# Performance work log

Hardware: AMD Instinct MI355X
Metric: run time of the kernel (lower is better)

## Reference

```python
import jax, jax.numpy as jnp
import numpy as np


def _layer_norm(x, g, b, eps=1e-5):
    mu = jnp.mean(x, axis=-1, keepdims=True)
    var = jnp.mean((x - mu) ** 2, axis=-1, keepdims=True)
    return (x - mu) * jax.lax.rsqrt(var + eps) * g + b


def setup_inputs() -> dict:
    key = jax.random.key(0)
    ks = jax.random.split(key, 12)
    L, D, HD, F, V, MAXLEN, B, S = 4, 1024, 64, 4096, 32000, 2048, 2, 1024
    s = 0.02
    return {
        "x": jax.random.randint(ks[0], (B, S), 0, V, dtype=jnp.int32),
        "tok_emb": jax.random.normal(ks[1], (V, D), jnp.float32) * s,
        "pos_emb": jax.random.normal(ks[2], (MAXLEN, D), jnp.float32) * s,
        "wq": jax.random.normal(ks[3], (L, HD, HD), jnp.float32) * s,
        "wk": jax.random.normal(ks[4], (L, HD, HD), jnp.float32) * s,
        "wv": jax.random.normal(ks[5], (L, HD, HD), jnp.float32) * s,
        "wo": jax.random.normal(ks[6], (L, D, D), jnp.float32) * s,
        "bo": jnp.zeros((L, D), jnp.float32),
        "ln1_g": jnp.ones((L, D), jnp.float32),
        "ln1_b": jnp.zeros((L, D), jnp.float32),
        "ln2_g": jnp.ones((L, D), jnp.float32),
        "ln2_b": jnp.zeros((L, D), jnp.float32),
        "w1": jax.random.normal(ks[7], (L, F, D), jnp.float32) * s,
        "b1": jnp.zeros((L, F), jnp.float32),
        "w2": jax.random.normal(ks[8], (L, D, F), jnp.float32) * s,
        "b2": jnp.zeros((L, D), jnp.float32),
        "out_w": jax.random.normal(ks[9], (V, D), jnp.float32) * s,
        "out_b": jnp.zeros((V,), jnp.float32),
    }


def reference(x, tok_emb, pos_emb, wq, wk, wv, wo, bo, ln1_g, ln1_b, ln2_g, ln2_b, w1, b1, w2, b2, out_w, out_b):
    B, S = x.shape
    D = tok_emb.shape[1]
    HD = wq.shape[-1]
    H = D // HD
    inv_scale = 1.0 / jnp.sqrt(jnp.asarray(D, jnp.float32))  # note: embed_size, not head_dim

    h = tok_emb[x] + pos_emb[:S][None]  # [B,S,D]; dropout is identity in eval

    def block(h, p):
        pwq, pwk, pwv, pwo, pbo, g1, be1, g2, be2, pw1, pb1, pw2, pb2 = p
        xh = h.reshape(B, S, H, HD)
        # per-head Linear with shared [HD,HD] weight: y = x @ W.T
        q = jnp.einsum('bshd,ed->bshe', xh, pwq)
        k = jnp.einsum('bshd,ed->bshe', xh, pwk)
        v = jnp.einsum('bshd,ed->bshe', xh, pwv)
        energy = jnp.einsum('bqhd,bkhd->bhqk', q, k)  # full [B,H,S,S] scores
        attn = jax.nn.softmax(energy * inv_scale, axis=-1)
        o = jnp.einsum('bhqk,bkhd->bqhd', attn, v).reshape(B, S, D)
        o = o @ pwo.T + pbo
        x1 = _layer_norm(o + h, g1, be1)
        ff = jax.nn.gelu(x1 @ pw1.T + pb1, approximate=False) @ pw2.T + pb2
        return _layer_norm(ff + x1, g2, be2), None

    h, _ = jax.lax.scan(block, h, (wq, wk, wv, wo, bo, ln1_g, ln1_b, ln2_g, ln2_b, w1, b1, w2, b2))
    return h @ out_w.T + out_b  # [B,S,V] logits
```

## Files before the change

kernel.cpp:

```cpp
#include <hip/hip_runtime.h>
#include <math.h>

typedef float f32x4 __attribute__((ext_vector_type(4)));
typedef unsigned short u16x8 __attribute__((ext_vector_type(8)));
typedef unsigned short u16x4 __attribute__((ext_vector_type(4)));
typedef __bf16 bf16x8 __attribute__((ext_vector_type(8)));
typedef unsigned int u32;

#define DEV static __device__ __forceinline__

DEV unsigned short f2bf(float f) {
  __bf16 h = (__bf16)f;
  return __builtin_bit_cast(unsigned short, h);
}
DEV float bf2f(unsigned short s) { return __uint_as_float(((unsigned)s) << 16); }
DEV bf16x8 asbf(u16x8 v) { return __builtin_bit_cast(bf16x8, v); }

DEV void gload16(const void* g, void* l) {
  __builtin_amdgcn_global_load_lds((const __attribute__((address_space(1))) u32*)g,
                                   (__attribute__((address_space(3))) u32*)l, 16, 0, 0);
}

__global__ void cvt_kernel(const float* __restrict__ in, unsigned short* __restrict__ out, int n8) {
  for (int i = blockIdx.x * 256 + threadIdx.x; i < n8; i += gridDim.x * 256) {
    const float* s = in + (size_t)i * 8;
    f32x4 a = *(const f32x4*)s, b = *(const f32x4*)(s + 4);
    u16x8 o;
    for (int j = 0; j < 4; ++j) { o[j] = f2bf(a[j]); o[j + 4] = f2bf(b[j]); }
    *(u16x8*)(out + (size_t)i * 8) = o;
  }
}

__global__ void cvt2_kernel(const float* __restrict__ s0, unsigned short* __restrict__ d0, int na,
                            const float* __restrict__ s1, unsigned short* __restrict__ d1, int nb) {
  int total = na + nb;
  for (int i = blockIdx.x * 256 + threadIdx.x; i < total; i += gridDim.x * 256) {
    const float* s; unsigned short* d; int k;
    if (i < na) { s = s0; d = d0; k = i; } else { s = s1; d = d1; k = i - na; }
    f32x4 a = *(const f32x4*)(s + (size_t)k * 8), b = *(const f32x4*)(s + (size_t)k * 8 + 4);
    u16x8 o;
    for (int j = 0; j < 4; ++j) { o[j] = f2bf(a[j]); o[j + 4] = f2bf(b[j]); }
    *(u16x8*)(d + (size_t)k * 8) = o;
  }
}

__global__ void cvt3q_kernel(const float* __restrict__ s0, unsigned short* __restrict__ d0,
                             const float* __restrict__ s1, unsigned short* __restrict__ d1,
                             const float* __restrict__ s2, unsigned short* __restrict__ d2) {
  int i = blockIdx.x * 256 + threadIdx.x;
  if (i >= 6144) return;
  const float* s; unsigned short* d; int k = i & 2047;
  int seg = i >> 11;
  s = (seg == 0) ? s0 : (seg == 1) ? s1 : s2;
  d = (seg == 0) ? d0 : (seg == 1) ? d1 : d2;
  f32x4 a = *(const f32x4*)(s + (size_t)k * 8), b = *(const f32x4*)(s + (size_t)k * 8 + 4);
  u16x8 o;
  for (int j = 0; j < 4; ++j) { o[j] = f2bf(a[j]); o[j + 4] = f2bf(b[j]); }
  *(u16x8*)(d + (size_t)k * 8) = o;
}

__global__ void embed_kernel(const int* __restrict__ x, const float* __restrict__ tok,
                             const float* __restrict__ pos, float* __restrict__ h,
                             unsigned short* __restrict__ hbf) {
  int t = blockIdx.x, tid = threadIdx.x;
  int v = x[t], s = t & 1023;
  f32x4 a = *(const f32x4*)(tok + (size_t)v * 1024 + tid * 4);
  f32x4 b = *(const f32x4*)(pos + (size_t)s * 1024 + tid * 4);
  f32x4 r = a + b;
  *(f32x4*)(h + (size_t)t * 1024 + tid * 4) = r;
  u16x4 rb;
  for (int i = 0; i < 4; ++i) rb[i] = f2bf(r[i]);
  *(u16x4*)(hbf + (size_t)t * 1024 + tid * 4) = rb;
}

__global__ __launch_bounds__(256) void ln_kernel(const float* __restrict__ preA,
    const float* __restrict__ preB, const float* __restrict__ res,
    const float* __restrict__ g, const float* __restrict__ bta,
    float* __restrict__ outf, unsigned short* __restrict__ outbf) {
  int row = blockIdx.x, tid = threadIdx.x;
  size_t base = (size_t)row * 1024 + tid * 4;
  f32x4 xv = *(const f32x4*)(preA + base);
  xv += *(const f32x4*)(preB + base);
  xv += *(const f32x4*)(res + base);
  float s = xv[0] + xv[1] + xv[2] + xv[3];
  float s2 = xv[0]*xv[0] + xv[1]*xv[1] + xv[2]*xv[2] + xv[3]*xv[3];
  for (int m = 1; m < 64; m <<= 1) { s += __shfl_xor(s, m); s2 += __shfl_xor(s2, m); }
  __shared__ float red[8];
  int w = tid >> 6;
  if ((tid & 63) == 0) { red[w * 2] = s; red[w * 2 + 1] = s2; }
  __syncthreads();
  s = red[0] + red[2] + red[4] + red[6];
  s2 = red[1] + red[3] + red[5] + red[7];
  float mu = s * (1.f / 1024.f);
  float var = s2 * (1.f / 1024.f) - mu * mu;
  float rs = rsqrtf(var + 1e-5f);
  f32x4 gv = *(const f32x4*)(g + tid * 4);
  f32x4 bv = *(const f32x4*)(bta + tid * 4);
  f32x4 o; u16x4 ob;
  for (int i = 0; i < 4; ++i) { o[i] = (xv[i] - mu) * rs * gv[i] + bv[i]; ob[i] = f2bf(o[i]); }
  *(f32x4*)(outf + base) = o;
  *(u16x4*)(outbf + base) = ob;
}

__global__ __launch_bounds__(256) void qkvt_kernel(const unsigned short* __restrict__ hbf,
    const unsigned short* __restrict__ wqb, const unsigned short* __restrict__ wkb,
    const unsigned short* __restrict__ wvb,
    unsigned short* __restrict__ q, unsigned short* __restrict__ k,
    unsigned short* __restrict__ vt) {
  __shared__ unsigned short T[64 * 72];
  int tid = threadIdx.x, ln = tid & 63, w = tid >> 6;
  int l15 = ln & 15, lg = ln >> 4;
  int st = blockIdx.x, hh = blockIdx.y;
  int t0 = st * 64 + w * 16;
  const unsigned short* xp = hbf + (size_t)(t0 + l15) * 1024 + hh * 64 + lg * 8;
  bf16x8 xa0 = asbf(*(const u16x8*)xp);
  bf16x8 xa1 = asbf(*(const u16x8*)(xp + 32));
  const unsigned short* wp[3] = {wqb, wkb, wvb};
  f32x4 acc[3][4] = {};
#pragma unroll
  for (int m = 0; m < 3; ++m) {
    __builtin_amdgcn_s_setprio(1);
#pragma unroll
    for (int ni = 0; ni < 4; ++ni) {
      const unsigned short* wb = wp[m] + (size_t)(ni * 16 + l15) * 64 + lg * 8;
      bf16x8 w0 = asbf(*(const u16x8*)wb);
      bf16x8 w1 = asbf(*(const u16x8*)(wb + 32));
      acc[m][ni] = __builtin_amdgcn_mfma_f32_16x16x32_bf16(xa0, w0, acc[m][ni], 0, 0, 0);
      acc[m][ni] = __builtin_amdgcn_mfma_f32_16x16x32_bf16(xa1, w1, acc[m][ni], 0, 0, 0);
    }
    __builtin_amdgcn_s_setprio(0);
  }
  unsigned short* outp[2] = {q, k};
#pragma unroll
  for (int m = 0; m < 2; ++m)
#pragma unroll
    for (int ni = 0; ni < 4; ++ni)
#pragma unroll
      for (int r = 0; r < 4; ++r)
        outp[m][(size_t)(t0 + 4 * lg + r) * 1024 + hh * 64 + ni * 16 + l15] = f2bf(acc[m][ni][r]);
#pragma unroll
  for (int ni = 0; ni < 4; ++ni)
#pragma unroll
    for (int r = 0; r < 4; ++r)
      T[(ni * 16 + l15) * 72 + (w * 16 + 4 * lg + r)] = f2bf(acc[2][ni][r]);
  __syncthreads();
  int b = st >> 4, sb = (st & 15) * 64;
#pragma unroll
  for (int j = 0; j < 2; ++j) {
    int idx = tid + 256 * j; int e = idx >> 3, s8 = (idx & 7) * 8;
    *(u16x8*)(vt + ((size_t)((b * 16 + hh) * 64 + e)) * 1024 + sb + s8) =
        *(const u16x8*)&T[e * 72 + s8];
  }
}

__global__ __launch_bounds__(256, 2) void attn_kernel(const unsigned short* __restrict__ qb,
    const unsigned short* __restrict__ kb, const unsigned short* __restrict__ vtb,
    unsigned short* __restrict__ ob) {
  constexpr int PK = 72, PV = 136, PP = 136;
  __shared__ unsigned short Ks[128 * PK], Vs[64 * PV], Ps[4][16 * PP];
  int tid = threadIdx.x, lane = tid & 63, w = tid >> 6;
  int l15 = lane & 15, lg = lane >> 4;
  int qt = blockIdx.x, bh = blockIdx.y, b = bh >> 4, hh = bh & 15;
  int q0 = qt * 64 + w * 16;
  const unsigned short* qrow = qb + ((size_t)(b * 1024 + q0 + l15) * 16 + hh) * 64 + lg * 8;
  bf16x8 qa0 = asbf(*(const u16x8*)qrow);
  bf16x8 qa1 = asbf(*(const u16x8*)(qrow + 32));
  {
    const __bf16 s = (__bf16)0.03125f;
#pragma unroll
    for (int i = 0; i < 8; ++i) { qa0[i] = qa0[i] * s; qa1[i] = qa1[i] * s; }
  }
  float m_[4] = {-1e30f, -1e30f, -1e30f, -1e30f};
  float ls[4] = {0.f, 0.f, 0.f, 0.f};
  f32x4 oacc[4] = {};

  u16x8 KR[4], VR[4];
  auto loadT = [&](int kt) {
#pragma unroll
    for (int j = 0; j < 4; ++j) {
      int idx = tid + 256 * j;
      int r = idx >> 3, c0 = (idx & 7) * 8;
      KR[j] = *(const u16x8*)(kb + ((size_t)(b * 1024 + kt * 128 + r) * 16 + hh) * 64 + c0);
      int rv = idx >> 4, cv = (idx & 15) * 8;
      VR[j] = *(const u16x8*)(vtb + ((size_t)((b * 16 + hh) * 64) + rv) * 1024 + kt * 128 + cv);
    }
  };
  auto writeT = [&]() {
#pragma unroll
    for (int j = 0; j < 4; ++j) {
      int idx = tid + 256 * j;
      int r = idx >> 3, c0 = (idx & 7) * 8;
      *(u16x8*)(&Ks[r * PK + c0]) = KR[j];
      int rv = idx >> 4, cv = (idx & 15) * 8;
      *(u16x8*)(&Vs[rv * PV + cv]) = VR[j];
    }
  };
  loadT(0); writeT();
  __syncthreads();

  for (int kt = 0; kt < 8; ++kt) {
    f32x4 sf[8] = {};
    __builtin_amdgcn_s_setprio(1);
#pragma unroll
    for (int n = 0; n < 8; ++n) {
      bf16x8 k0 = asbf(*(const u16x8*)(&Ks[(n * 16 + l15) * PK + lg * 8]));
      bf16x8 k1 = asbf(*(const u16x8*)(&Ks[(n * 16 + l15) * PK + 32 + lg * 8]));
      sf[n] = __builtin_amdgcn_mfma_f32_16x16x32_bf16(qa0, k0, sf[n], 0, 0, 0);
      sf[n] = __builtin_amdgcn_mfma_f32_16x16x32_bf16(qa1, k1, sf[n], 0, 0, 0);
    }
    __builtin_amdgcn_s_setprio(0);
    if (kt < 7) loadT(kt + 1);
    float tm[4];
#pragma unroll
    for (int r = 0; r < 4; ++r) {
      float t0 = fmaxf(fmaxf(fmaxf(sf[0][r], sf[1][r]), fmaxf(sf[2][r], sf[3][r])),
                       fmaxf(fmaxf(sf[4][r], sf[5][r]), fmaxf(sf[6][r], sf[7][r])));
      for (int msk = 1; msk < 16; msk <<= 1) t0 = fmaxf(t0, __shfl_xor(t0, msk));
      tm[r] = t0;
    }
    bool need = false;
#pragma unroll
    for (int r = 0; r < 4; ++r) need |= (tm[r] > m_[r] + 8.f);
    if (__any(need)) {
#pragma unroll
      for (int r = 0; r < 4; ++r) {
        float nm = fmaxf(m_[r], tm[r]);
        float sc = __expf(m_[r] - nm);
        ls[r] *= sc;
#pragma unroll
        for (int n = 0; n < 4; ++n) oacc[n][r] *= sc;
        m_[r] = nm;
      }
    }
    float rsum[4] = {0.f, 0.f, 0.f, 0.f};
    unsigned short pb[8][4];
#pragma unroll
    for (int n = 0; n < 8; ++n)
#pragma unroll
      for (int r = 0; r < 4; ++r) {
        float pv = __expf(sf[n][r] - m_[r]);
        rsum[r] += pv;
        pb[n][r] = f2bf(pv);
      }
#pragma unroll
    for (int r = 0; r < 4; ++r) {
      float t0 = rsum[r];
      for (int msk = 1; msk < 16; msk <<= 1) t0 += __shfl_xor(t0, msk);
      ls[r] += t0;
    }
    unsigned short* pw = Ps[w];
#pragma unroll
    for (int n = 0; n < 8; ++n)
#pragma unroll
      for (int r = 0; r < 4; ++r)
        pw[(4 * lg + r) * PP + n * 16 + l15] = pb[n][r];
    asm volatile("s_waitcnt lgkmcnt(0)" ::: "memory");
    __builtin_amdgcn_sched_barrier(0);
    bf16x8 pa[4];
#pragma unroll
    for (int ks = 0; ks < 4; ++ks)
      pa[ks] = asbf(*(const u16x8*)(&pw[l15 * PP + ks * 32 + lg * 8]));
    __builtin_amdgcn_s_setprio(1);
#pragma unroll
    for (int n = 0; n < 4; ++n) {
#pragma unroll
      for (int ks = 0; ks < 4; ++ks) {
        bf16x8 v0 = asbf(*(const u16x8*)(&Vs[(n * 16 + l15) * PV + ks * 32 + lg * 8]));
        oacc[n] = __builtin_amdgcn_mfma_f32_16x16x32_bf16(pa[ks], v0, oacc[n], 0, 0, 0);
      }
    }
    __builtin_amdgcn_s_setprio(0);
    __syncthreads();
    if (kt < 7) { writeT(); __syncthreads(); }
  }
#pragma unroll
  for (int n = 0; n < 4; ++n)
#pragma unroll
    for (int r = 0; r < 4; ++r) {
      float o = oacc[n][r] / ls[r];
      ob[((size_t)(b * 1024 + q0 + 4 * lg + r) * 16 + hh) * 64 + n * 16 + l15] = f2bf(o);
    }
}

template <int BM, int KSPLIT, int EPI>
__global__ __launch_bounds__(256) void gemm_kernel(
    const unsigned short* __restrict__ A, int lda,
    const unsigned short* __restrict__ B, int ldb,
    const float* __restrict__ bias,
    float* __restrict__ CfA, float* __restrict__ CfB, unsigned short* __restrict__ Cb,
    int ldc, int Ksub) {
  constexpr int LOGMT = (BM == 128) ? 4 : 5;
  constexpr int MT = 2048 / BM;
  constexpr int MI = BM / 32;
  __shared__ alignas(16) char smem[33280];
  unsigned short* As = (unsigned short*)smem;
  unsigned short* Bs = As + 2 * BM * 32;
  float* Cs = (float*)smem;

  int wg = blockIdx.x;
  int mt = wg & (MT - 1);
  int rest = wg >> LOGMT;
  int nt, kh;
  if (KSPLIT == 2) { nt = rest & 7; kh = rest >> 3; }
  else { nt = rest; kh = 0; }
  int m0 = mt * BM, n0 = nt * 128;
  const unsigned short* Ae = A + (KSPLIT == 2 ? (size_t)kh * Ksub : 0);
  const unsigned short* Be = B + (KSPLIT == 2 ? (size_t)kh * Ksub : 0);

  int tid = threadIdx.x, ln = tid & 63, wv = tid >> 6;
  int l15 = ln & 15, lg = ln >> 4;
  int wm = (wv >> 1) * (BM / 2), wn = (wv & 1) * 64;

  auto stage = [&](int buf, int k0) {
    for (int j = 0; j < BM / 64; ++j) {
      int row = j * 64 + wv * 16 + (ln >> 2);
      gload16(Ae + (size_t)(m0 + row) * lda + k0 + (ln & 3) * 8,
              &As[buf * (BM * 32) + (j * 64 + wv * 16) * 32]);
    }
    for (int j = 0; j < 2; ++j) {
      int row = j * 64 + wv * 16 + (ln >> 2);
      gload16(Be + (size_t)(n0 + row) * ldb + k0 + (ln & 3) * 8,
              &Bs[buf * 4096 + (j * 64 + wv * 16) * 32]);
    }
  };

  f32x4 acc[MI][4] = {};
  auto compute = [&](int buf) {
    const unsigned short* as = &As[buf * (BM * 32)];
    const unsigned short* bs = &Bs[buf * 4096];
    bf16x8 af[MI], bfn[4];
    for (int mi = 0; mi < MI; ++mi)
      af[mi] = asbf(*(const u16x8*)&as[(wm + mi * 16 + l15) * 32 + lg * 8]);
    for (int ni = 0; ni < 4; ++ni)
      bfn[ni] = asbf(*(const u16x8*)&bs[(wn + ni * 16 + l15) * 32 + lg * 8]);
    for (int mi = 0; mi < MI; ++mi)
      for (int ni = 0; ni < 4; ++ni)
        acc[mi][ni] = __builtin_amdgcn_mfma_f32_16x16x32_bf16(af[mi], bfn[ni], acc[mi][ni], 0, 0, 0);
  };

  stage(0, 0);
  __syncthreads();
  int ntk = Ksub >> 5, cur = 0;
  for (int t = 0; t < ntk - 1; ++t) {
    stage(cur ^ 1, (t + 1) << 5);
    compute(cur);
    __syncthreads();
    cur ^= 1;
  }
  compute(cur);

  float* Cf = (kh == 0) ? CfA : CfB;
  const bool addb = (kh == 0);
  for (int p = 0; p < BM / 64; ++p) {
    __syncthreads();
    if ((wm >> 6) == p) {
      int rb = wm & 63;
      for (int mi = 0; mi < MI; ++mi)
        for (int ni = 0; ni < 4; ++ni) {
          int cn = wn + ni * 16 + l15;
          float bv = addb ? bias[n0 + cn] : 0.f;
          for (int r = 0; r < 4; ++r) {
            float vv = acc[mi][ni][r] + bv;
            if (EPI == 1) vv = 0.5f * vv * (1.f + erff(vv * 0.70710678118f));
            Cs[(rb + mi * 16 + 4 * lg + r) * 130 + cn] = vv;
          }
        }
    }
    __syncthreads();
    int row = tid >> 3;
    for (int ri = 0; ri < 2; ++ri) {
      int lr = ri * 32 + row;
      size_t gbase = (size_t)(m0 + p * 64 + lr) * ldc + n0;
      if (EPI == 0) {
        int c4 = (tid & 7) * 4;
        for (int j = 0; j < 4; ++j)
          *(f32x4*)(Cf + gbase + c4 + j * 32) = *(const f32x4*)&Cs[lr * 130 + c4 + j * 32];
      } else {
        for (int j = 0; j < 2; ++j) {
          int cc = (tid & 7) * 8 + j * 64;
          f32x4 v0 = *(const f32x4*)&Cs[lr * 130 + cc];
          f32x4 v1 = *(const f32x4*)&Cs[lr * 130 + cc + 4];
          u16x8 o;
          for (int i = 0; i < 4; ++i) { o[i] = f2bf(v0[i]); o[i + 4] = f2bf(v1[i]); }
          *(u16x8*)(Cb + gbase + cc) = o;
        }
      }
    }
  }
}

__global__ __launch_bounds__(512, 1) void gemmF1_kernel(
    const unsigned short* __restrict__ A, int lda,
    const unsigned short* __restrict__ B, int ldb,
    const float* __restrict__ bias, unsigned short* __restrict__ Cb, int ldc, int K) {
  extern __shared__ unsigned short sm[];
  int b = blockIdx.x;
  int c = (int)gridDim.x >> 3;
  int wg = (b & 7) * c + (b >> 3);
  int mt = wg & 15, nt = wg >> 4;
  int m0 = mt * 128, n0 = nt * 256;

  int tid = threadIdx.x, ln = tid & 63, wv = tid >> 6;
  int l15 = ln & 15, lg = ln >> 4;
  int wm = wv >> 2, wn = wv & 3;
  int l7 = l15 & 7;

  int srow = tid >> 3, sblk = (tid & 7) ^ (srow & 7);
  const unsigned short* Ab = A + (size_t)(m0 + srow) * lda + sblk * 8;
  const unsigned short* BbG[4];
#pragma unroll
  for (int g = 0; g < 4; ++g) {
    int p = g * 64 + srow;
    int j = p & 127;
    int r = ((j >> 5) << 6) + ((p >> 7) << 5) + (j & 31);
    BbG[g] = B + (size_t)(n0 + r) * ldb + sblk * 8;
  }
  auto stA = [&](int e, int g, int k0) {
    gload16(Ab + ((size_t)g * 64) * lda + k0, &sm[e * 8192 + g * 4096 + wv * 512]);
  };
  auto stB = [&](int e, int g, int k0) {
    gload16(BbG[g] + k0, &sm[16384 + e * 16384 + g * 4096 + wv * 512]);
  };

  auto ldsA = [&](int d, int mi, int ks) -> bf16x8 {
    int row = wm * 64 + mi * 16 + l15;
    return asbf(*(const u16x8*)&sm[d * 8192 + row * 64 + (((ks << 2) | lg) ^ l7) * 8]);
  };
  auto ldsB = [&](int d, int ni, int ks) -> bf16x8 {
    int p = ((ni >> 1) << 7) + wn * 32 + ((ni & 1) << 4) + l15;
    return asbf(*(const u16x8*)&sm[16384 + d * 16384 + p * 64 + (((ks << 2) | lg) ^ l7) * 8]);
  };

  f32x4 acc[4][4] = {};
  bf16x8 Af[4][2], Bf01[2][2], Bf23[2][2];

#define PH_OPEN() __builtin_amdgcn_s_barrier(); \
  asm volatile("s_waitcnt lgkmcnt(0)" ::: "memory"); \
  __builtin_amdgcn_sched_barrier(0); __builtin_amdgcn_s_setprio(1)

  stA(0, 0, 0); stA(0, 1, 0); stB(0, 0, 0); stB(0, 1, 0);
  stB(0, 2, 0); stB(0, 3, 0);
  asm volatile("s_waitcnt vmcnt(2)" ::: "memory");
  __builtin_amdgcn_s_barrier();

  int ntk = K >> 6;
  for (int kk = 0; kk < ntk; ++kk) {
    int d = kk & 1, e = d ^ 1, k1 = (kk + 1) << 6;
    bool pf = (kk + 1 < ntk);
    {
#pragma unroll
      for (int ni = 0; ni < 2; ++ni) { Bf01[ni][0] = ldsB(d, ni, 0); Bf01[ni][1] = ldsB(d, ni, 1); }
#pragma unroll
      for (int mi = 0; mi < 4; ++mi) { Af[mi][0] = ldsA(d, mi, 0); Af[mi][1] = ldsA(d, mi, 1); }
      if (pf) { stA(e, 0, k1); stA(e, 1, k1); stB(e, 0, k1); stB(e, 1, k1); }
      PH_OPEN();
#pragma unroll
      for (int mi = 0; mi < 4; ++mi)
#pragma unroll
        for (int ni = 0; ni < 2; ++ni) {
          acc[mi][ni] = __builtin_amdgcn_mfma_f32_16x16x32_bf16(Af[mi][0], Bf01[ni][0], acc[mi][ni], 0, 0, 0);
          acc[mi][ni] = __builtin_amdgcn_mfma_f32_16x16x32_bf16(Af[mi][1], Bf01[ni][1], acc[mi][ni], 0, 0, 0);
        }
      __builtin_amdgcn_s_setprio(0);
      if (pf) { asm volatile("s_waitcnt vmcnt(4)" ::: "memory"); }
      else    { asm volatile("s_waitcnt vmcnt(0)" ::: "memory"); }
      __builtin_amdgcn_s_barrier();
    }
    {
#pragma unroll
      for (int ni = 0; ni < 2; ++ni) { Bf23[ni][0] = ldsB(d, 2 + ni, 0); Bf23[ni][1] = ldsB(d, 2 + ni, 1); }
      if (pf) { stB(e, 2, k1); stB(e, 3, k1); }
      PH_OPEN();
#pragma unroll
      for (int mi = 0; mi < 4; ++mi)
#pragma unroll
        for (int ni = 0; ni < 2; ++ni) {
          acc[mi][2 + ni] = __builtin_amdgcn_mfma_f32_16x16x32_bf16(Af[mi][0], Bf23[ni][0], acc[mi][2 + ni], 0, 0, 0);
          acc[mi][2 + ni] = __builtin_amdgcn_mfma_f32_16x16x32_bf16(Af[mi][1], Bf23[ni][1], acc[mi][2 + ni], 0, 0, 0);
        }
      __builtin_amdgcn_s_setprio(0);
      if (pf) { asm volatile("s_waitcnt vmcnt(2)" ::: "memory"); }
      __builtin_amdgcn_s_barrier();
    }
  }
#undef PH_OPEN

  float* fb = (float*)sm;
  int fbase = wv * 4096;
  float bv[4];
#pragma unroll
  for (int ni = 0; ni < 4; ++ni) bv[ni] = bias[n0 + wn * 64 + ni * 16 + l15];
#pragma unroll
  for (int mi = 0; mi < 4; ++mi)
#pragma unroll
    for (int ni = 0; ni < 4; ++ni)
#pragma unroll
      for (int r = 0; r < 4; ++r) {
        float vv = acc[mi][ni][r] + bv[ni];
        vv = 0.5f * vv * (1.f + erff(vv * 0.70710678118f));
        fb[fbase + (mi * 16 + lg * 4 + r) * 64 + ni * 16 + l15] = vv;
      }
  asm volatile("s_waitcnt lgkmcnt(0)" ::: "memory");
  __builtin_amdgcn_sched_barrier(0);
#pragma unroll
  for (int i = 0; i < 8; ++i) {
    int row = i * 8 + (ln >> 3);
    int cc = (ln & 7) * 8;
    f32x4 v0 = *(const f32x4*)&fb[fbase + row * 64 + cc];
    f32x4 v1 = *(const f32x4*)&fb[fbase + row * 64 + cc + 4];
    u16x8 o;
#pragma unroll
    for (int j = 0; j < 4; ++j) { o[j] = f2bf(v0[j]); o[j + 4] = f2bf(v1[j]); }
    *(u16x8*)(Cb + (size_t)(m0 + wm * 64 + row) * ldc + n0 + wn * 64 + cc) = o;
  }
}

__global__ __launch_bounds__(512, 1) void gemm256_kernel(
    const unsigned short* __restrict__ A, int lda,
    const unsigned short* __restrict__ B, int ldb,
    const float* __restrict__ bias, float* __restrict__ C, int ldc, int K) {
  extern __shared__ unsigned short sm[];
  int b = blockIdx.x;
  int c = (int)gridDim.x >> 3;
  int wg = (b & 7) * c + (b >> 3);
  int mt = wg & 7, nt = wg >> 3;
  int m0 = mt * 256, n0 = nt * 256;

  int tid = threadIdx.x, ln = tid & 63, wv = tid >> 6;
  int l15 = ln & 15, lg = ln >> 4;
  int wm = wv >> 2, wn = wv & 3;
  int l7 = l15 & 7;

  int srow = tid >> 3, sblk = (tid & 7) ^ (srow & 7);
  const unsigned short* Ab = A + (size_t)(m0 + srow) * lda + sblk * 8;
  const unsigned short* BbG[4];
#pragma unroll
  for (int g = 0; g < 4; ++g) {
    int p = g * 64 + srow;
    int j = p & 127;
    int r = ((j >> 5) << 6) + ((p >> 7) << 5) + (j & 31);
    BbG[g] = B + (size_t)(n0 + r) * ldb + sblk * 8;
  }
  auto stA = [&](int e, int g, int k0) {
    gload16(Ab + ((size_t)g * 64) * lda + k0, &sm[e * 16384 + g * 4096 + wv * 512]);
  };
  auto stB = [&](int e, int g, int k0) {
    gload16(BbG[g] + k0, &sm[32768 + e * 16384 + g * 4096 + wv * 512]);
  };

  auto ldsA = [&](int d, int mi, int ks) -> bf16x8 {
    int row = wm * 128 + mi * 16 + l15;
    return asbf(*(const u16x8*)&sm[d * 16384 + row * 64 + (((ks << 2) | lg) ^ l7) * 8]);
  };
  auto ldsB = [&](int d, int ni, int ks) -> bf16x8 {
    int p = ((ni >> 1) << 7) + wn * 32 + ((ni & 1) << 4) + l15;
    return asbf(*(const u16x8*)&sm[32768 + d * 16384 + p * 64 + (((ks << 2) | lg) ^ l7) * 8]);
  };

  f32x4 acc[8][4] = {};
  bf16x8 Af[4][2], Bf01[2][2], Bf23[2][2];

#define PH_OPEN() __builtin_amdgcn_s_barrier(); \
  asm volatile("s_waitcnt lgkmcnt(0)" ::: "memory"); \
  __builtin_amdgcn_sched_barrier(0); __builtin_amdgcn_s_setprio(1)

  stA(0, 0, 0); stA(0, 2, 0); stB(0, 0, 0); stB(0, 1, 0);
  stB(0, 2, 0); stB(0, 3, 0); stA(0, 1, 0); stA(0, 3, 0);
  asm volatile("s_waitcnt vmcnt(0)" ::: "memory");
  __builtin_amdgcn_s_barrier();

  int ntk = K >> 6;
  for (int kk = 0; kk < ntk; ++kk) {
    int d = kk & 1, e = d ^ 1, k1 = (kk + 1) << 6;
    bool pf = (kk + 1 < ntk);
    {
#pragma unroll
      for (int ni = 0; ni < 2; ++ni) { Bf01[ni][0] = ldsB(d, ni, 0); Bf01[ni][1] = ldsB(d, ni, 1); }
#pragma unroll
      for (int mi = 0; mi < 4; ++mi) { Af[mi][0] = ldsA(d, mi, 0); Af[mi][1] = ldsA(d, mi, 1); }
      if (pf) { stA(e, 0, k1); stA(e, 2, k1); stB(e, 0, k1); stB(e, 1, k1); }
      PH_OPEN();
#pragma unroll
      for (int mi = 0; mi < 4; ++mi)
#pragma unroll
        for (int ni = 0; ni < 2; ++ni) {
          acc[mi][ni] = __builtin_amdgcn_mfma_f32_16x16x32_bf16(Af[mi][0], Bf01[ni][0], acc[mi][ni], 0, 0, 0);
          acc[mi][ni] = __builtin_amdgcn_mfma_f32_16x16x32_bf16(Af[mi][1], Bf01[ni][1], acc[mi][ni], 0, 0, 0);
        }
      __builtin_amdgcn_s_setprio(0);
      if (pf) { asm volatile("s_waitcnt vmcnt(6)" ::: "memory"); }
      else    { asm volatile("s_waitcnt vmcnt(2)" ::: "memory"); }
      __builtin_amdgcn_s_barrier();
    }
    {
#pragma unroll
      for (int ni = 0; ni < 2; ++ni) { Bf23[ni][0] = ldsB(d, 2 + ni, 0); Bf23[ni][1] = ldsB(d, 2 + ni, 1); }
      if (pf) { stB(e, 2, k1); stB(e, 3, k1); }
      PH_OPEN();
#pragma unroll
      for (int mi = 0; mi < 4; ++mi)
#pragma unroll
        for (int ni = 0; ni < 2; ++ni) {
          acc[mi][2 + ni] = __builtin_amdgcn_mfma_f32_16x16x32_bf16(Af[mi][0], Bf23[ni][0], acc[mi][2 + ni], 0, 0, 0);
          acc[mi][2 + ni] = __builtin_amdgcn_mfma_f32_16x16x32_bf16(Af[mi][1], Bf23[ni][1], acc[mi][2 + ni], 0, 0, 0);
        }
      __builtin_amdgcn_s_setprio(0);
      if (pf) { asm volatile("s_waitcnt vmcnt(6)" ::: "memory"); }
      else    { asm volatile("s_waitcnt vmcnt(0)" ::: "memory"); }
      __builtin_amdgcn_s_barrier();
    }
    {
#pragma unroll
      for (int mi = 0; mi < 4; ++mi) { Af[mi][0] = ldsA(d, 4 + mi, 0); Af[mi][1] = ldsA(d, 4 + mi, 1); }
      if (pf) { stA(e, 1, k1); stA(e, 3, k1); }
      PH_OPEN();
#pragma unroll
      for (int mi = 0; mi < 4; ++mi)
#pragma unroll
        for (int ni = 0; ni < 2; ++ni) {
          acc[4 + mi][2 + ni] = __builtin_amdgcn_mfma_f32_16x16x32_bf16(Af[mi][0], Bf23[ni][0], acc[4 + mi][2 + ni], 0, 0, 0);
          acc[4 + mi][2 + ni] = __builtin_amdgcn_mfma_f32_16x16x32_bf16(Af[mi][1], Bf23[ni][1], acc[4 + mi][2 + ni], 0, 0, 0);
        }
      __builtin_amdgcn_s_setprio(0);
      __builtin_amdgcn_s_barrier();
    }
    {
      PH_OPEN();
#pragma unroll
      for (int mi = 0; mi < 4; ++mi)
#pragma unroll
        for (int ni = 0; ni < 2; ++ni) {
          acc[4 + mi][ni] = __builtin_amdgcn_mfma_f32_16x16x32_bf16(Af[mi][0], Bf01[ni][0], acc[4 + mi][ni], 0, 0, 0);
          acc[4 + mi][ni] = __builtin_amdgcn_mfma_f32_16x16x32_bf16(Af[mi][1], Bf01[ni][1], acc[4 + mi][ni], 0, 0, 0);
        }
      __builtin_amdgcn_s_setprio(0);
      if (pf) { asm volatile("s_waitcnt vmcnt(4)" ::: "memory"); }
      __builtin_amdgcn_s_barrier();
    }
  }
#undef PH_OPEN

  float* fb = (float*)sm;
  int fbase = wv * 4096;
  float bv[4];
#pragma unroll
  for (int ni = 0; ni < 4; ++ni) bv[ni] = bias[n0 + wn * 64 + ni * 16 + l15];
#pragma unroll
  for (int p = 0; p < 2; ++p) {
    if (p) { asm volatile("s_waitcnt lgkmcnt(0)" ::: "memory"); __builtin_amdgcn_sched_barrier(0); }
#pragma unroll
    for (int mi = 0; mi < 4; ++mi)
#pragma unroll
      for (int ni = 0; ni < 4; ++ni)
#pragma unroll
        for (int r = 0; r < 4; ++r)
          fb[fbase + (mi * 16 + lg * 4 + r) * 64 + ni * 16 + l15] = acc[4 * p + mi][ni][r] + bv[ni];
    asm volatile("s_waitcnt lgkmcnt(0)" ::: "memory");
    __builtin_amdgcn_sched_barrier(0);
#pragma unroll
    for (int i = 0; i < 16; ++i) {
      int row = i * 4 + lg;
      f32x4 v = *(const f32x4*)&fb[fbase + row * 64 + l15 * 4];
      int grow = m0 + wm * 128 + p * 64 + row;
      *(f32x4*)(&C[(size_t)grow * ldc + n0 + wn * 64 + l15 * 4]) = v;
    }
  }
}

extern "C" void kernel_launch(void* const* d_in, const int* in_sizes, int n_in,
                              void* d_out, int out_size, void* d_ws, size_t ws_size,
                              hipStream_t stream) {
  const int* x = (const int*)d_in[0];
  const float* tok = (const float*)d_in[1];
  const float* pos = (const float*)d_in[2];
  const float* wq = (const float*)d_in[3];
  const float* wk = (const float*)d_in[4];
  const float* wv = (const float*)d_in[5];
  const float* wo = (const float*)d_in[6];
  const float* bo = (const float*)d_in[7];
  const float* ln1g = (const float*)d_in[8];
  const float* ln1b = (const float*)d_in[9];
  const float* ln2g = (const float*)d_in[10];
  const float* ln2b = (const float*)d_in[11];
  const float* w1 = (const float*)d_in[12];
  const float* b1 = (const float*)d_in[13];
  const float* w2 = (const float*)d_in[14];
  const float* b2 = (const float*)d_in[15];
  const float* outw = (const float*)d_in[16];
  const float* outb = (const float*)d_in[17];
  float* out = (float*)d_out;

  const size_t MiB = 1 << 20;
  const size_t need = 4 * MiB + 65536000;
  if (ws_size < need) return;
  char* base = (char*)d_ws;
  unsigned short* hbf = (unsigned short*)base;
  char* R = base + 4 * MiB;
  float* hf  = (float*)(R);
  float* x1f = (float*)(R + 8 * MiB);
  unsigned short* x1bf = (unsigned short*)(R + 16 * MiB);
  float* cfA = (float*)(R + 20 * MiB);
  float* cfB = (float*)(R + 28 * MiB);
  unsigned short* qs = (unsigned short*)(R + 36 * MiB);
  const size_t SL = 2048ull * 1024;
  unsigned short* qbf = qs;
  unsigned short* kbf = qs + SL;
  unsigned short* vbf = qs + 2 * SL;
  unsigned short* vtbf = qs + 3 * SL;
  unsigned short* wobf = vtbf;
  unsigned short* w1bf = qbf;
  unsigned short* w2bf = qbf;
  unsigned short* ffbf = vbf;
  unsigned short* wqbf = (unsigned short*)(R + 60 * MiB);
  unsigned short* wkbf = wqbf + 16384;
  unsigned short* wvbf = wkbf + 16384;
  unsigned short* outwbf = (unsigned short*)R;

  embed_kernel<<<2048, 256, 0, stream>>>(x, tok, pos, hf, hbf);
  cvt3q_kernel<<<24, 256, 0, stream>>>(wq, wqbf, wk, wkbf, wv, wvbf);
  for (int l = 0; l < 4; ++l) {
    qkvt_kernel<<<dim3(32, 16), 256, 0, stream>>>(hbf, wqbf + l * 4096, wkbf + l * 4096,
                                                  wvbf + l * 4096, qbf, kbf, vtbf);
    attn_kernel<<<dim3(16, 32), 256, 0, stream>>>(qbf, kbf, vtbf, vbf);
    cvt2_kernel<<<2048, 256, 0, stream>>>(wo + (size_t)l * 1048576, wobf, 131072,
                                          w1 + (size_t)l * 4194304, w1bf, 524288);
    gemm_kernel<64, 2, 0><<<512, 256, 0, stream>>>(
        vbf, 1024, wobf, 1024, bo + l * 1024, cfA, cfB, nullptr, 1024, 512);
    ln_kernel<<<2048, 256, 0, stream>>>(cfA, cfB, hf, ln1g + l * 1024, ln1b + l * 1024,
                                        x1f, x1bf);
    gemmF1_kernel<<<256, 512, 131072, stream>>>(
        x1bf, 1024, w1bf, 1024, b1 + l * 4096, ffbf, 4096, 1024);
    cvt_kernel<<<2048, 256, 0, stream>>>(w2 + (size_t)l * 4194304, w2bf, 524288);
    gemm_kernel<64, 2, 0><<<512, 256, 0, stream>>>(
        ffbf, 4096, w2bf, 4096, b2 + l * 1024, cfA, cfB, nullptr, 1024, 2048);
    ln_kernel<<<2048, 256, 0, stream>>>(cfA, cfB, x1f, ln2g + l * 1024, ln2b + l * 1024,
                                        hf, hbf);
  }
  cvt_kernel<<<2048, 256, 0, stream>>>(outw, outwbf, 4096000);
  gemm256_kernel<<<1000, 512, 131072, stream>>>(hbf, 1024, outwbf, 1024, outb, out, 32000, 1024);
}
```

Baseline: 810.5 us.

## Replace split-K output GEMM with 64x256-tile swizzled pipelined GEMM kernel

Swaps the generic 64x128 split-K GEMM used for the attention output projection and the FFN down projection for a new 512-thread kernel. It uses 64x256 tiles with K-step 64, XOR-swizzled LDS layouts and two-phase interleaving of global-to-LDS prefetch with MFMA under explicit waitcnt and barriers. It also adds an XCD-aware block remap and a per-wave LDS-staged fp32 epilogue. The aim is better operand reuse, fewer LDS bank conflicts and more overlap of loads with compute. The cost is fewer workgroups (256) and more LDS per block, which may reduce occupancy.

```diff
diff --git a/kernel.cpp b/kernel.cpp
--- a/kernel.cpp
+++ b/kernel.cpp
@@ -282,110 +282,117 @@
     }
 }
 
-template <int BM, int KSPLIT, int EPI>
-__global__ __launch_bounds__(256) void gemm_kernel(
+__global__ __launch_bounds__(512, 2) void gemmF2_kernel(
     const unsigned short* __restrict__ A, int lda,
     const unsigned short* __restrict__ B, int ldb,
     const float* __restrict__ bias,
-    float* __restrict__ CfA, float* __restrict__ CfB, unsigned short* __restrict__ Cb,
-    int ldc, int Ksub) {
-  constexpr int LOGMT = (BM == 128) ? 4 : 5;
-  constexpr int MT = 2048 / BM;
-  constexpr int MI = BM / 32;
-  __shared__ alignas(16) char smem[33280];
-  unsigned short* As = (unsigned short*)smem;
-  unsigned short* Bs = As + 2 * BM * 32;
-  float* Cs = (float*)smem;
-
-  int wg = blockIdx.x;
-  int mt = wg & (MT - 1);
-  int rest = wg >> LOGMT;
-  int nt, kh;
-  if (KSPLIT == 2) { nt = rest & 7; kh = rest >> 3; }
-  else { nt = rest; kh = 0; }
-  int m0 = mt * BM, n0 = nt * 128;
-  const unsigned short* Ae = A + (KSPLIT == 2 ? (size_t)kh * Ksub : 0);
-  const unsigned short* Be = B + (KSPLIT == 2 ? (size_t)kh * Ksub : 0);
+    float* __restrict__ CfA, float* __restrict__ CfB, int Ksub) {
+  extern __shared__ unsigned short sm[];
+  int b = blockIdx.x;
+  int c = (int)gridDim.x >> 3;
+  int wg = (b & 7) * c + (b >> 3);
+  int mt = wg & 31, nt = (wg >> 5) & 3, kh = wg >> 7;
+  int m0 = mt * 64, n0 = nt * 256;
+  const unsigned short* Ae = A + (size_t)kh * Ksub;
+  const unsigned short* Be = B + (size_t)kh * Ksub;
 
   int tid = threadIdx.x, ln = tid & 63, wv = tid >> 6;
   int l15 = ln & 15, lg = ln >> 4;
-  int wm = (wv >> 1) * (BM / 2), wn = (wv & 1) * 64;
-
-  auto stage = [&](int buf, int k0) {
-    for (int j = 0; j < BM / 64; ++j) {
-      int row = j * 64 + wv * 16 + (ln >> 2);
-      gload16(Ae + (size_t)(m0 + row) * lda + k0 + (ln & 3) * 8,
-              &As[buf * (BM * 32) + (j * 64 + wv * 16) * 32]);
-    }
-    for (int j = 0; j < 2; ++j) {
-      int row = j * 64 + wv * 16 + (ln >> 2);
-      gload16(Be + (size_t)(n0 + row) * ldb + k0 + (ln & 3) * 8,
-              &Bs[buf * 4096 + (j * 64 + wv * 16) * 32]);
-    }
-  };
-
-  f32x4 acc[MI][4] = {};
-  auto compute = [&](int buf) {
-    const unsigned short* as = &As[buf * (BM * 32)];
-    const unsigned short* bs = &Bs[buf * 4096];
-    bf16x8 af[MI], bfn[4];
-    for (int mi = 0; mi < MI; ++mi)
-      af[mi] = asbf(*(const u16x8*)&as[(wm + mi * 16 + l15) * 32 + lg * 8]);
-    for (int ni = 0; ni < 4; ++ni)
-      bfn[ni] = asbf(*(const u16x8*)&bs[(wn + ni * 16 + l15) * 32 + lg * 8]);
-    for (int mi = 0; mi < MI; ++mi)
-      for (int ni = 0; ni < 4; ++ni)
-        acc[mi][ni] = __builtin_amdgcn_mfma_f32_16x16x32_bf16(af[mi], bfn[ni], acc[mi][ni], 0, 0, 0);
-  };
-
-  stage(0, 0);
-  __syncthreads();
-  int ntk = Ksub >> 5, cur = 0;
-  for (int t = 0; t < ntk - 1; ++t) {
-    stage(cur ^ 1, (t + 1) << 5);
-    compute(cur);
-    __syncthreads();
-    cur ^= 1;
-  }
-  compute(cur);
-
+  int wn = wv;
+  int l7 = l15 & 7;
+
+  int srow = tid >> 3, sblk = (tid & 7) ^ (srow & 7);
+  const unsigned short* Ab = Ae + (size_t)(m0 + srow) * lda + sblk * 8;
+  const unsigned short* BbG[4];
+#pragma unroll
+  for (int g = 0; g < 4; ++g) {
+    int p = g * 64 + srow;
+    int f = p >> 7, wnn = (p >> 4) & 7;
+    int r = wnn * 32 + f * 16 + (p & 15);
+    BbG[g] = Be + (size_t)(n0 + r) * ldb + sblk * 8;
+  }
+  auto stA = [&](int e, int k0) {
+    gload16(Ab + k0, &sm[e * 4096 + wv * 512]);
+  };
+  auto stB = [&](int e, int g, int k0) {
+    gload16(BbG[g] + k0, &sm[8192 + e * 16384 + g * 4096 + wv * 512]);
+  };
+  auto ldsA = [&](int d, int mi, int ks) -> bf16x8 {
+    int row = mi * 16 + l15;
+    return asbf(*(const u16x8*)&sm[d * 4096 + row * 64 + (((ks << 2) | lg) ^ l7) * 8]);
+  };
+  auto ldsB = [&](int d, int f, int ks) -> bf16x8 {
+    int p = f * 128 + wn * 16 + l15;
+    return asbf(*(const u16x8*)&sm[8192 + d * 16384 + p * 64 + (((ks << 2) | lg) ^ l7) * 8]);
+  };
+
+  f32x4 acc[4][2] = {};
+  bf16x8 Af[4][2], Bf0[2], Bf1[2];
+
+#define PH_OPEN() __builtin_amdgcn_s_barrier(); \
+  asm volatile("s_waitcnt lgkmcnt(0)" ::: "memory"); \
+  __builtin_amdgcn_sched_barrier(0); __builtin_amdgcn_s_setprio(1)
+
+  stA(0, 0); stB(0, 0, 0); stB(0, 1, 0); stB(0, 2, 0); stB(0, 3, 0);
+  asm volatile("s_waitcnt vmcnt(2)" ::: "memory");
+  __builtin_amdgcn_s_barrier();
+
+  int ntk = Ksub >> 6;
+  for (int kk = 0; kk < ntk; ++kk) {
+    int d = kk & 1, e = d ^ 1, k1 = (kk + 1) << 6;
+    bool pf = (kk + 1 < ntk);
+    {
+      Bf0[0] = ldsB(d, 0, 0); Bf0[1] = ldsB(d, 0, 1);
+#pragma unroll
+      for (int mi = 0; mi < 4; ++mi) { Af[mi][0] = ldsA(d, mi, 0); Af[mi][1] = ldsA(d, mi, 1); }
+      if (pf) { stA(e, k1); stB(e, 0, k1); stB(e, 1, k1); }
+      PH_OPEN();
+#pragma unroll
+      for (int mi = 0; mi < 4; ++mi) {
+        acc[mi][0] = __builtin_amdgcn_mfma_f32_16x16x32_bf16(Af[mi][0], Bf0[0], acc[mi][0], 0, 0, 0);
+        acc[mi][0] = __builtin_amdgcn_mfma_f32_16x16x32_bf16(Af[mi][1], Bf0[1], acc[mi][0], 0, 0, 0);
+      }
+      __builtin_amdgcn_s_setprio(0);
+      if (pf) { asm volatile("s_waitcnt vmcnt(3)" ::: "memory"); }
+      else    { asm volatile("s_waitcnt vmcnt(0)" ::: "memory"); }
+      __builtin_amdgcn_s_barrier();
+    }
+    {
+      Bf1[0] = ldsB(d, 1, 0); Bf1[1] = ldsB(d, 1, 1);
+      if (pf) { stB(e, 2, k1); stB(e, 3, k1); }
+      PH_OPEN();
+#pragma unroll
+      for (int mi = 0; mi < 4; ++mi) {
+        acc[mi][1] = __builtin_amdgcn_mfma_f32_16x16x32_bf16(Af[mi][0], Bf1[0], acc[mi][1], 0, 0, 0);
+        acc[mi][1] = __builtin_amdgcn_mfma_f32_16x16x32_bf16(Af[mi][1], Bf1[1], acc[mi][1], 0, 0, 0);
+      }
+      __builtin_amdgcn_s_setprio(0);
+      if (pf) { asm volatile("s_waitcnt vmcnt(2)" ::: "memory"); }
+      __builtin_amdgcn_s_barrier();
+    }
+  }
+#undef PH_OPEN
+
+  float* fb = (float*)sm;
+  int fbase = wv * 2048;
   float* Cf = (kh == 0) ? CfA : CfB;
-  const bool addb = (kh == 0);
-  for (int p = 0; p < BM / 64; ++p) {
-    __syncthreads();
-    if ((wm >> 6) == p) {
-      int rb = wm & 63;
-      for (int mi = 0; mi < MI; ++mi)
-        for (int ni = 0; ni < 4; ++ni) {
-          int cn = wn + ni * 16 + l15;
-          float bv = addb ? bias[n0 + cn] : 0.f;
-          for (int r = 0; r < 4; ++r) {
-            float vv = acc[mi][ni][r] + bv;
-            if (EPI == 1) vv = 0.5f * vv * (1.f + erff(vv * 0.70710678118f));
-            Cs[(rb + mi * 16 + 4 * lg + r) * 130 + cn] = vv;
-          }
-        }
-    }
-    __syncthreads();
-    int row = tid >> 3;
-    for (int ri = 0; ri < 2; ++ri) {
-      int lr = ri * 32 + row;
-      size_t gbase = (size_t)(m0 + p * 64 + lr) * ldc + n0;
-      if (EPI == 0) {
-        int c4 = (tid & 7) * 4;
-        for (int j = 0; j < 4; ++j)
-          *(f32x4*)(Cf + gbase + c4 + j * 32) = *(const f32x4*)&Cs[lr * 130 + c4 + j * 32];
-      } else {
-        for (int j = 0; j < 2; ++j) {
-          int cc = (tid & 7) * 8 + j * 64;
-          f32x4 v0 = *(const f32x4*)&Cs[lr * 130 + cc];
-          f32x4 v1 = *(const f32x4*)&Cs[lr * 130 + cc + 4];
-          u16x8 o;
-          for (int i = 0; i < 4; ++i) { o[i] = f2bf(v0[i]); o[i + 4] = f2bf(v1[i]); }
-          *(u16x8*)(Cb + gbase + cc) = o;
-        }
-      }
-    }
+  float bv[2] = {0.f, 0.f};
+  if (kh == 0) { bv[0] = bias[n0 + wn * 32 + l15]; bv[1] = bias[n0 + wn * 32 + 16 + l15]; }
+#pragma unroll
+  for (int mi = 0; mi < 4; ++mi)
+#pragma unroll
+    for (int f = 0; f < 2; ++f)
+#pragma unroll
+      for (int r = 0; r < 4; ++r)
+        fb[fbase + (mi * 16 + lg * 4 + r) * 32 + f * 16 + l15] = acc[mi][f][r] + bv[f];
+  asm volatile("s_waitcnt lgkmcnt(0)" ::: "memory");
+  __builtin_amdgcn_sched_barrier(0);
+#pragma unroll
+  for (int i = 0; i < 8; ++i) {
+    int row = i * 8 + (ln >> 3);
+    int col = (ln & 7) * 4;
+    f32x4 v = *(const f32x4*)&fb[fbase + row * 32 + col];
+    *(f32x4*)(&Cf[(size_t)(m0 + row) * 1024 + n0 + wn * 32 + col]) = v;
   }
 }
 
@@ -724,15 +731,15 @@
     attn_kernel<<<dim3(16, 32), 256, 0, stream>>>(qbf, kbf, vtbf, vbf);
     cvt2_kernel<<<2048, 256, 0, stream>>>(wo + (size_t)l * 1048576, wobf, 131072,
                                           w1 + (size_t)l * 4194304, w1bf, 524288);
-    gemm_kernel<64, 2, 0><<<512, 256, 0, stream>>>(
-        vbf, 1024, wobf, 1024, bo + l * 1024, cfA, cfB, nullptr, 1024, 512);
+    gemmF2_kernel<<<256, 512, 81920, stream>>>(
+        vbf, 1024, wobf, 1024, bo + l * 1024, cfA, cfB, 512);
     ln_kernel<<<2048, 256, 0, stream>>>(cfA, cfB, hf, ln1g + l * 1024, ln1b + l * 1024,
                                         x1f, x1bf);
     gemmF1_kernel<<<256, 512, 131072, stream>>>(
         x1bf, 1024, w1bf, 1024, b1 + l * 4096, ffbf, 4096, 1024);
     cvt_kernel<<<2048, 256, 0, stream>>>(w2 + (size_t)l * 4194304, w2bf, 524288);
-    gemm_kernel<64, 2, 0><<<512, 256, 0, stream>>>(
-        ffbf, 4096, w2bf, 4096, b2 + l * 1024, cfA, cfB, nullptr, 1024, 2048);
+    gemmF2_kernel<<<256, 512, 81920, stream>>>(
+        ffbf, 4096, w2bf, 4096, b2 + l * 1024, cfA, cfB, 2048);
     ln_kernel<<<2048, 256, 0, stream>>>(cfA, cfB, x1f, ln2g + l * 1024, ln2b + l * 1024,
                                         hf, hbf);
   }
```

Result: faster. 765.1 us (median of 3 runs) (-5.6%).
